# Kernel optimization log

Hardware: AMD Instinct MI355X
Metric: run time of the kernel (lower is better)

The kernel has to match this reference:

```python
import jax, jax.numpy as jnp
import numpy as np
from jax import lax

N = 20          # PARAM.N discretization steps
STEP_SIZE = 1.0 / N  # max_T / N = 1 / 20
B = 1_048_576   # number of Monte-Carlo paths


def _lin_init(key, fan_in, fan_out):
    kw, kb = jax.random.split(key)
    s = 1.0 / np.sqrt(fan_in)
    W = jax.random.uniform(kw, (fan_in, fan_out), minval=-s, maxval=s, dtype=jnp.float32)
    b = jax.random.uniform(kb, (fan_out,), minval=-s, maxval=s, dtype=jnp.float32)
    return W, b


def setup_inputs() -> dict:
    key = jax.random.key(0)
    ks = jax.random.split(key, 10)
    S0 = jax.random.uniform(ks[0], (B,), minval=50.0, maxval=150.0, dtype=jnp.float32)
    K = jax.random.uniform(ks[1], (B,), minval=50.0, maxval=150.0, dtype=jnp.float32)
    # maturities in {0.5, 1.0} per PARAM.maturities
    T = jnp.where(jax.random.bernoulli(ks[2], 0.5, (B,)), 0.5, 1.0).astype(jnp.float32)
    BM = jax.random.normal(ks[3], (B, N), dtype=jnp.float32)
    # 3 stacks: (4->30->5), (5->30->5), (5->30->2)
    W1, b1 = _lin_init(ks[4], 4, 30)
    W2, b2 = _lin_init(ks[5], 30, 5)
    W3, b3 = _lin_init(ks[6], 5, 30)
    W4, b4 = _lin_init(ks[7], 30, 5)
    W5, b5 = _lin_init(ks[8], 5, 30)
    W6, b6 = _lin_init(ks[9], 30, 2)
    return dict(S0=S0, K=K, T=T, BM=BM,
                W1=W1, b1=b1, W2=W2, b2=b2, W3=W3, b3=b3,
                W4=W4, b4=b4, W5=W5, b5=b5, W6=W6, b6=b6)


def reference(S0, K, T, BM, W1, b1, W2, b2, W3, b3, W4, b4, W5, b5, W6, b6):
    def net(x):  # [B,4] -> [B,2]
        h = jax.nn.relu(x @ W1 + b1) @ W2 + b2
        h = jax.nn.relu(h @ W3 + b3) @ W4 + b4
        return jax.nn.relu(h @ W5 + b5) @ W6 + b6

    def feats(price, time):  # [B,4] features: price, time, T-time, log(price/K)
        t = time * jnp.ones_like(price)
        return jnp.stack([price, t, T - t, jnp.log(price / K)], axis=-1)

    def step(carry, inp):
        price, hedgepf = carry
        idx, dW = inp
        time = (idx + 1.0) / N
        do_comp = (time <= T).astype(price.dtype)
        inc = dW * STEP_SIZE
        lev = net(feats(price, time))[:, 0]
        price = price + do_comp * lev * price * inc
        hed = net(feats(price, time))[:, 1] * inc
        hedgepf = hedgepf + do_comp * hed
        return (price, hedgepf), None

    init = (S0, jnp.zeros_like(S0))
    xs = (jnp.arange(N, dtype=S0.dtype), BM.T)  # scan over time steps
    (price, hedgepf), _ = lax.scan(step, init, xs)
    payoff = (price - K + jnp.abs(price - K)) * 0.5  # == relu(price - K)
    return payoff - hedgepf
```

## Files before the change

### kernel.cpp

```cpp
#include <hip/hip_runtime.h>

#define NSTEPS 20

typedef short bf16x8 __attribute__((ext_vector_type(8)));
typedef float f32x16 __attribute__((ext_vector_type(16)));

union B8 { bf16x8 h; unsigned u[4]; unsigned short s[8]; };

__device__ __forceinline__ unsigned short f2bf(float x) {
    unsigned u = __builtin_bit_cast(unsigned, x);
    u += 0x7fffu + ((u >> 16) & 1u);
    return (unsigned short)(u >> 16);
}
__device__ __forceinline__ float bf2f(unsigned short b) {
    return __builtin_bit_cast(float, (unsigned)b << 16);
}
__device__ __forceinline__ unsigned pk(unsigned short lo, unsigned short hi) {
    return (unsigned)lo | ((unsigned)hi << 16);
}
__device__ __forceinline__ unsigned cvtpk(float a, float b) {
    unsigned r;
    asm("v_cvt_pk_bf16_f32 %0, %1, %2" : "=v"(r) : "v"(a), "v"(b));
    return r;
}
__device__ __forceinline__ float lo_f(unsigned w) { return __builtin_bit_cast(float, w << 16); }
__device__ __forceinline__ float hi_f(unsigned w) { return __builtin_bit_cast(float, w & 0xffff0000u); }

#define MFMA(A, B, C) __builtin_amdgcn_mfma_f32_32x32x16_bf16((A), (B), (C), 0, 0, 0)
#define PRIO1() __builtin_amdgcn_s_setprio(1)
#define PRIO0() __builtin_amdgcn_s_setprio(0)

__device__ __forceinline__ void wlimbs(float w, unsigned short& l0, unsigned short& l1, unsigned short& l2) {
    l0 = f2bf(w); float e = w - bf2f(l0);
    l1 = f2bf(e); e -= bf2f(l1);
    l2 = f2bf(e);
}
__device__ __forceinline__ unsigned short pick(int m, unsigned short l0, unsigned short l1, unsigned short l2) {
    return (m == 0) ? l0 : ((m == 1) ? l1 : l2);
}


template<int F_, int M>
__device__ __forceinline__ bf16x8 awide(const float* W, const float* bias, int nout, int ld, int lane)
{
    const int u = lane & 31, h = (lane >> 5) & 1;
    B8 r;
#pragma unroll
    for (int j = 0; j < 8; ++j) {
        const int k = 16 * F_ + 4 * h + (j & 3) + 8 * (j >> 2);
        float v = 0.f;
        if (u < nout) {
            if (k < 30) v = W[k * ld + u];
            else if (k == 30) v = bias[u];
        }
        unsigned short l0, l1, l2; wlimbs(v, l0, l1, l2);
        r.s[j] = (short)pick(M, l0, l1, l2);
    }
    return r.h;
}

template<int S, int F_>
__device__ __forceinline__ bf16x8 a5(const float* W, const float* bias, int lane)
{
    const int u = lane & 31, h = (lane >> 5) & 1;
    B8 r;
#pragma unroll
    for (int j = 0; j < 8; ++j) {
        const int k = 16 * F_ + 4 * h + (j & 3) + 8 * (j >> 2);
        unsigned short bits = 0;
        if (u < 30) {
            int in = -1, m = -1;
            if (F_ == 0) {
                if (k < 4)       { in = k; m = S; }
                else if (k == 4) { in = 4; m = S; }
            } else {
                if (k >= 16 && k < 20)      { in = k - 16; m = (S == 0) ? 1 : ((S == 1) ? 0 : -1); }
                else if (k == 20)           { in = 4;      m = (S == 0) ? 1 : ((S == 1) ? 0 : -1); }
                else if (k >= 24 && k < 28) { in = k - 24; m = (S == 0) ? 2 : ((S == 2) ? 0 : -1); }
                else if (k == 21)           { in = 4;      m = (S == 0) ? 2 : ((S == 2) ? 0 : -1); }
            }
            if (in >= 0 && m >= 0) {
                unsigned short l0, l1, l2; wlimbs(W[in * 30 + u], l0, l1, l2);
                bits = pick(m, l0, l1, l2);
            } else if (F_ == 0 && k == 15) {
                unsigned short l0, l1, l2; wlimbs(bias[u], l0, l1, l2);
                bits = pick(S, l0, l1, l2);
            }
        }
        r.s[j] = (short)bits;
    }
    return r.h;
}

template<int S>
__device__ __forceinline__ bf16x8 a1f(const float* W1, const float* b1v, int lane)
{
    const int perm[4] = {0, 3, 1, 2};
    const int u = lane & 31, h = (lane >> 5) & 1;
    B8 r;
#pragma unroll
    for (int j = 0; j < 8; ++j) {
        const int k = 4 * h + (j & 3) + 8 * (j >> 2);
        unsigned short bits = 0;
        if (u < 30) {
            int in = -1, m = -1;
            if (k < 4)       { in = k;     m = (S == 0) ? 0 : ((S == 1) ? 1 : 2); }
            else if (k < 8)  { in = k - 4; m = (S == 0) ? 1 : ((S == 1) ? 0 : -1); }
            else if (k < 12) { in = k - 8; m = (S == 0) ? 2 : ((S == 2) ? 0 : -1); }
            if (in >= 0 && m >= 0) {
                unsigned short l0, l1, l2; wlimbs(W1[perm[in] * 30 + u], l0, l1, l2);
                bits = pick(m, l0, l1, l2);
            } else if (k == 12) {
                unsigned short l0, l1, l2; wlimbs(b1v[u], l0, l1, l2);
                bits = pick(S, l0, l1, l2);
            }
        }
        r.s[j] = (short)bits;
    }
    return r.h;
}


template<int LIMBS>
__device__ __forceinline__ void split_pair(float a, float b,
                                           unsigned& w0, unsigned& w1, unsigned& w2)
{
    w0 = cvtpk(a, b);
    if (LIMBS >= 2) {
        float e0 = a - lo_f(w0), e1 = b - hi_f(w0);
        w1 = cvtpk(e0, e1);
        if (LIMBS == 3) {
            float f0 = e0 - lo_f(w1), f1 = e1 - hi_f(w1);
            w2 = cvtpk(f0, f1);
        } else w2 = 0u;
    } else { w1 = 0u; w2 = 0u; }
}

template<int LIMBS>
__device__ __forceinline__ void split30(const f32x16& acc, bool hi,
                                        B8& B0a, B8& B0b, B8& B1a, B8& B1b,
                                        B8& B2a, B8& B2b)
{
#pragma unroll
    for (int i = 0; i < 4; ++i) {
        const float a = fmaxf(acc[2 * i], 0.f), b = fmaxf(acc[2 * i + 1], 0.f);
        unsigned w0, w1, w2; split_pair<LIMBS>(a, b, w0, w1, w2);
        B0a.u[i] = w0;
        if (LIMBS >= 2) B1a.u[i] = w1;
        if (LIMBS == 3) B2a.u[i] = w2;
    }
#pragma unroll
    for (int i = 0; i < 4; ++i) {
        const float a = fmaxf(acc[8 + 2 * i], 0.f), b = fmaxf(acc[8 + 2 * i + 1], 0.f);
        unsigned w0, w1, w2; split_pair<LIMBS>(a, b, w0, w1, w2);
        B0b.u[i] = w0;
        if (LIMBS >= 2) B1b.u[i] = w1;
        if (LIMBS == 3) B2b.u[i] = w2;
    }
    if (hi) {
        B0b.u[3] = 0x00003F80u;
        if (LIMBS >= 2) B1b.u[3] = 0u;
        if (LIMBS == 3) B2b.u[3] = 0u;
    }
}

template<int LIMBS>
__device__ __forceinline__ void split5(const f32x16& acc, bool hi, B8& C0, B8& C1)
{
    const float a0 = acc[0], a1 = acc[1];
    const float a2 = acc[2], a3 = acc[3];
    unsigned p0, p1, p2, q0, q1, q2;
    split_pair<LIMBS>(a0, a1, p0, p1, p2);
    split_pair<LIMBS>(a2, a3, q0, q1, q2);
    if (!hi) {
        C0.u[0] = p0; C0.u[1] = q0; C0.u[2] = 0; C0.u[3] = 0;
        if (LIMBS >= 2) {
            C1.u[0] = p1; C1.u[1] = q1;
            C1.u[2] = (LIMBS == 3) ? p2 : 0u;
            C1.u[3] = (LIMBS == 3) ? q2 : 0u;
        }
    } else {
        C0.u[0] = p0 & 0xffffu;
        C0.u[1] = 0; C0.u[2] = 0;
        C0.u[3] = 0x3F800000u;
        if (LIMBS >= 2) {
            C1.u[0] = (LIMBS == 3) ? pk((unsigned short)(p1 & 0xffffu), (unsigned short)(p2 & 0xffffu))
                                   : (p1 & 0xffffu);
            C1.u[1] = 0; C1.u[2] = 0; C1.u[3] = 0;
        }
    }
}

struct Frags {
    bf16x8 A1_0, A1_1, A1_2;
    bf16x8 A2_00, A2_01, A2_10, A2_11, A2_20, A2_21;
    bf16x8 A3_00, A3_01, A3_10, A3_11, A3_20, A3_21;
    bf16x8 A4_00, A4_01, A4_10, A4_11, A4_20, A4_21;
    bf16x8 A5_00, A5_01, A5_10, A5_11, A5_20, A5_21;
};

template<int LIMBS>
__device__ __forceinline__ f32x16 evalnet5(
    float price, float f3, unsigned tT0, unsigned tT1, unsigned tT2,
    bool hi, const Frags& F, const f32x16& Z)
{
    unsigned pf0, pf1, pf2;
    split_pair<LIMBS>(price, f3, pf0, pf1, pf2);
    B8 B;
    if (!hi) {
        B.u[0] = pf0; B.u[1] = tT0;
        B.u[2] = (LIMBS == 3) ? pf2 : 0u;
        B.u[3] = (LIMBS == 3) ? tT2 : 0u;
    } else {
        B.u[0] = (LIMBS >= 2) ? pf1 : 0u;
        B.u[1] = (LIMBS >= 2) ? tT1 : 0u;
        B.u[2] = 0x00003F80u;
        B.u[3] = 0u;
    }

    PRIO1();
    f32x16 acc = MFMA(F.A1_0, B.h, Z);
    if (LIMBS >= 2) acc = MFMA(F.A1_1, B.h, acc);
    if (LIMBS == 3) acc = MFMA(F.A1_2, B.h, acc);
    PRIO0();

    B8 B0a, B0b, B1a, B1b, B2a, B2b, C0, C1;
    f32x16 p, q;

    split30<LIMBS>(acc, hi, B0a, B0b, B1a, B1b, B2a, B2b);
    PRIO1();
    p = MFMA(F.A2_00, B0a.h, Z);
    q = MFMA(F.A2_01, B0b.h, Z);
    if (LIMBS >= 2) {
        p = MFMA(F.A2_00, B1a.h, p);
        q = MFMA(F.A2_01, B1b.h, q);
        if (LIMBS == 3) { p = MFMA(F.A2_00, B2a.h, p); q = MFMA(F.A2_01, B2b.h, q); }
        p = MFMA(F.A2_10, B0a.h, p);
        q = MFMA(F.A2_11, B0b.h, q);
        p = MFMA(F.A2_10, B1a.h, p);
        q = MFMA(F.A2_11, B1b.h, q);
        if (LIMBS == 3) { p = MFMA(F.A2_20, B0a.h, p); q = MFMA(F.A2_21, B0b.h, q); }
    }
    PRIO0();
    acc = p + q;

    split5<LIMBS>(acc, hi, C0, C1);
    PRIO1();
    if (LIMBS >= 2) {
        p = MFMA(F.A3_00, C0.h, Z);
        q = MFMA(F.A3_01, C1.h, Z);
        p = MFMA(F.A3_10, C0.h, p);
        q = MFMA(F.A3_11, C1.h, q);
        if (LIMBS == 3) { p = MFMA(F.A3_20, C0.h, p); q = MFMA(F.A3_21, C1.h, q); }
        acc = p + q;
    } else {
        acc = MFMA(F.A3_00, C0.h, Z);
    }
    PRIO0();

    split30<LIMBS>(acc, hi, B0a, B0b, B1a, B1b, B2a, B2b);
    PRIO1();
    p = MFMA(F.A4_00, B0a.h, Z);
    q = MFMA(F.A4_01, B0b.h, Z);
    if (LIMBS >= 2) {
        p = MFMA(F.A4_00, B1a.h, p);
        q = MFMA(F.A4_01, B1b.h, q);
        if (LIMBS == 3) { p = MFMA(F.A4_00, B2a.h, p); q = MFMA(F.A4_01, B2b.h, q); }
        p = MFMA(F.A4_10, B0a.h, p);
        q = MFMA(F.A4_11, B0b.h, q);
        p = MFMA(F.A4_10, B1a.h, p);
        q = MFMA(F.A4_11, B1b.h, q);
        if (LIMBS == 3) { p = MFMA(F.A4_20, B0a.h, p); q = MFMA(F.A4_21, B0b.h, q); }
    }
    PRIO0();
    acc = p + q;

    split5<LIMBS>(acc, hi, C0, C1);
    PRIO1();
    if (LIMBS >= 2) {
        p = MFMA(F.A5_00, C0.h, Z);
        q = MFMA(F.A5_01, C1.h, Z);
        p = MFMA(F.A5_10, C0.h, p);
        q = MFMA(F.A5_11, C1.h, q);
        if (LIMBS == 3) { p = MFMA(F.A5_20, C0.h, p); q = MFMA(F.A5_21, C1.h, q); }
        acc = p + q;
    } else {
        acc = MFMA(F.A5_00, C0.h, Z);
    }
    PRIO0();

    return acc;
}

__global__ __launch_bounds__(1024) void partition_kernel(
    const float* __restrict__ Tv, int* __restrict__ ws, int Btot)
{
    __shared__ int cntA[16], cntB[16], baseSh[2];
    const int tid = threadIdx.x;
    const int wid = tid >> 6;
    const int lane = tid & 63;
    const int i = blockIdx.x * 1024 + tid;
    const bool valid = i < Btot;
    const bool isLong  = valid && (Tv[valid ? i : 0] > 0.75f);
    const bool isShort = valid && !isLong;
    const unsigned long long mA = __ballot(isLong);
    const unsigned long long mB = __ballot(isShort);
    const unsigned long long ltm = (1ull << lane) - 1ull;

    if (lane == 0) { cntA[wid] = __popcll(mA); cntB[wid] = __popcll(mB); }
    __syncthreads();
    if (tid == 0) {
        int ta = 0, tb = 0;
#pragma unroll
        for (int k = 0; k < 16; ++k) {
            const int a = cntA[k]; cntA[k] = ta; ta += a;
            const int b = cntB[k]; cntB[k] = tb; tb += b;
        }
        baseSh[0] = ta ? atomicAdd(&ws[0], ta) : 0;
        baseSh[1] = tb ? atomicAdd(&ws[1], tb) : 0;
    }
    __syncthreads();

    int* list = ws + 16;
    if (isLong) {
        const int pos = baseSh[0] + cntA[wid] + __popcll(mA & ltm);
        list[pos] = i;
    }
    if (isShort) {
        const int pos = baseSh[1] + cntB[wid] + __popcll(mB & ltm);
        list[Btot - 1 - pos] = i;
    }
}

template<int LIST>
__global__ __launch_bounds__(256) __attribute__((amdgpu_waves_per_eu(2, 3)))
void mc_hedge_mfma(
    const float* __restrict__ S0, const float* __restrict__ Kv,
    const float* __restrict__ Tv, const float* __restrict__ BM,
    const float* __restrict__ W1, const float* __restrict__ b1,
    const float* __restrict__ W2, const float* __restrict__ b2,
    const float* __restrict__ W3, const float* __restrict__ b3,
    const float* __restrict__ W4, const float* __restrict__ b4,
    const float* __restrict__ W5, const float* __restrict__ b5,
    const float* __restrict__ W6, const float* __restrict__ b6,
    const int* __restrict__ list, float* __restrict__ out, int Btot)
{
    const int lane = threadIdx.x & 63;
    const int wid  = threadIdx.x >> 6;
    const int base = blockIdx.x * 128 + wid * 32;
    if (base >= Btot) return;
    const int li = min(base + (lane & 31), Btot - 1);
    const int p = LIST ? list[li] : li;
    const bool hi = lane >= 32;

    Frags F;
    F.A1_0 = a1f<0>(W1, b1, lane);
    F.A1_1 = a1f<1>(W1, b1, lane);
    F.A1_2 = a1f<2>(W1, b1, lane);
    F.A2_00 = awide<0,0>(W2, b2, 5, 5, lane); F.A2_01 = awide<1,0>(W2, b2, 5, 5, lane);
    F.A2_10 = awide<0,1>(W2, b2, 5, 5, lane); F.A2_11 = awide<1,1>(W2, b2, 5, 5, lane);
    F.A2_20 = awide<0,2>(W2, b2, 5, 5, lane); F.A2_21 = awide<1,2>(W2, b2, 5, 5, lane);
    F.A3_00 = a5<0,0>(W3, b3, lane); F.A3_01 = a5<0,1>(W3, b3, lane);
    F.A3_10 = a5<1,0>(W3, b3, lane); F.A3_11 = a5<1,1>(W3, b3, lane);
    F.A3_20 = a5<2,0>(W3, b3, lane); F.A3_21 = a5<2,1>(W3, b3, lane);
    F.A4_00 = awide<0,0>(W4, b4, 5, 5, lane); F.A4_01 = awide<1,0>(W4, b4, 5, 5, lane);
    F.A4_10 = awide<0,1>(W4, b4, 5, 5, lane); F.A4_11 = awide<1,1>(W4, b4, 5, 5, lane);
    F.A4_20 = awide<0,2>(W4, b4, 5, 5, lane); F.A4_21 = awide<1,2>(W4, b4, 5, 5, lane);
    F.A5_00 = a5<0,0>(W5, b5, lane); F.A5_01 = a5<0,1>(W5, b5, lane);
    F.A5_10 = a5<1,0>(W5, b5, lane); F.A5_11 = a5<1,1>(W5, b5, lane);
    F.A5_20 = a5<2,0>(W5, b5, lane); F.A5_21 = a5<2,1>(W5, b5, lane);

    f32x16 wv0, wv1;
#pragma unroll
    for (int r = 0; r < 16; ++r) {
        const int row0 = (r & 3) + 8 * (r >> 2);
        const int row1 = row0 + 4;
        const float w00 = W6[row0 * 2 + 0];
        const float w01 = W6[row0 * 2 + 1];
        const float w10 = (row1 < 30) ? W6[row1 * 2 + 0] : 0.f;
        const float w11 = (row1 < 30) ? W6[row1 * 2 + 1] : 0.f;
        wv0[r] = hi ? w10 : w00;
        wv1[r] = hi ? w11 : w01;
    }
    const float b60 = b6[0], b61 = b6[1];

    f32x16 Z;
#pragma unroll
    for (int i = 0; i < 16; ++i) Z[i] = 0.0f;

    float price = S0[p];
    const float Kk = Kv[p];
    const float T  = Tv[p];
    const float logK = __logf(Kk);
    float hedge = 0.0f;
    const float* bmrow = BM + (size_t)p * NSTEPS;

    int wsteps = NSTEPS;
    if (LIST) {
        const int st = (T > 0.75f) ? NSTEPS : (NSTEPS / 2);
        wsteps = __shfl(st, 0);
    }

#pragma unroll 1
    for (int idx = 0; idx < wsteps; ++idx) {
        const float time = (float)(idx + 1) / (float)NSTEPS;
        const float docomp = (time <= T) ? 1.0f : 0.0f;
        const float inc = bmrow[idx] * (1.0f / (float)NSTEPS);
        const float tmt = T - time;

        unsigned tT0, tT1, tT2;
        split_pair<3>(time, tmt, tT0, tT1, tT2);

        float f3 = __logf(price) - logK;
        f32x16 a5v = evalnet5<3>(price, f3, tT0, tT1, tT2, hi, F, Z);
        float part = 0.f;
#pragma unroll
        for (int r = 0; r < 16; ++r) part = fmaf(fmaxf(a5v[r], 0.f), wv0[r], part);
        part += __shfl_xor(part, 32);
        const float lev = part + b60;
        price = price + docomp * lev * price * inc;

        f3 = __logf(price) - logK;
        a5v = evalnet5<1>(price, f3, tT0, tT1, tT2, hi, F, Z);
        part = 0.f;
#pragma unroll
        for (int r = 0; r < 16; ++r) part = fmaf(fmaxf(a5v[r], 0.f), wv1[r], part);
        part += __shfl_xor(part, 32);
        const float hed = (part + b61) * inc;
        hedge = hedge + docomp * hed;
    }

    if (!hi && (base + lane) < Btot) {
        const float payoff = fmaxf(price - Kk, 0.0f);
        out[p] = payoff - hedge;
    }
}

extern "C" void kernel_launch(void* const* d_in, const int* in_sizes, int n_in,
                              void* d_out, int out_size, void* d_ws, size_t ws_size,
                              hipStream_t stream)
{
    const float* S0 = (const float*)d_in[0];
    const float* Kv = (const float*)d_in[1];
    const float* Tv = (const float*)d_in[2];
    const float* BM = (const float*)d_in[3];
    const float* W1 = (const float*)d_in[4];
    const float* b1 = (const float*)d_in[5];
    const float* W2 = (const float*)d_in[6];
    const float* b2 = (const float*)d_in[7];
    const float* W3 = (const float*)d_in[8];
    const float* b3 = (const float*)d_in[9];
    const float* W4 = (const float*)d_in[10];
    const float* b4 = (const float*)d_in[11];
    const float* W5 = (const float*)d_in[12];
    const float* b5 = (const float*)d_in[13];
    const float* W6 = (const float*)d_in[14];
    const float* b6 = (const float*)d_in[15];

    float* out = (float*)d_out;
    const int B = in_sizes[0];
    const int gridC = (B + 127) / 128;
    const size_t need = (size_t)(16 + B) * sizeof(int);

    if (ws_size >= need) {
        int* ws = (int*)d_ws;
        hipMemsetAsync(ws, 0, 16 * sizeof(int), stream);
        partition_kernel<<<(B + 1023) / 1024, 1024, 0, stream>>>(Tv, ws, B);
        mc_hedge_mfma<1><<<gridC, 256, 0, stream>>>(
            S0, Kv, Tv, BM, W1, b1, W2, b2, W3, b3, W4, b4, W5, b5, W6, b6,
            ws + 16, out, B);
    } else {
        mc_hedge_mfma<0><<<gridC, 256, 0, stream>>>(
            S0, Kv, Tv, BM, W1, b1, W2, b2, W3, b3, W4, b4, W5, b5, W6, b6,
            (const int*)nullptr, out, B);
    }
}
```

Measured before the change: 869.7 us.

## Stage MFMA weight fragments in LDS and raise waves-per-EU target

The 27 bf16x8 weight fragments, previously held in registers by every wave, are now built once per block by wave 0 into shared memory and read from LDS at each MFMA. The waves_per_eu hint goes from (2,3) to (3,4) to use the freed registers for more resident waves and better latency hiding. The cost is an LDS read (ds_read_b128) before every MFMA in the inner loop, plus a block-wide barrier at start, which may add latency or contend on LDS bandwidth.

Result: faster. 712.4 us (-18.1%).

```diff
diff --git a/kernel.cpp b/kernel.cpp
--- a/kernel.cpp
+++ b/kernel.cpp
@@ -191,18 +191,12 @@
     }
 }
 
-struct Frags {
-    bf16x8 A1_0, A1_1, A1_2;
-    bf16x8 A2_00, A2_01, A2_10, A2_11, A2_20, A2_21;
-    bf16x8 A3_00, A3_01, A3_10, A3_11, A3_20, A3_21;
-    bf16x8 A4_00, A4_01, A4_10, A4_11, A4_20, A4_21;
-    bf16x8 A5_00, A5_01, A5_10, A5_11, A5_20, A5_21;
-};
+#define NFRAG 27
 
 template<int LIMBS>
 __device__ __forceinline__ f32x16 evalnet5(
     float price, float f3, unsigned tT0, unsigned tT1, unsigned tT2,
-    bool hi, const Frags& F, const f32x16& Z)
+    bool hi, const bf16x8* LF, int lane, const f32x16& Z)
 {
     unsigned pf0, pf1, pf2;
     split_pair<LIMBS>(price, f3, pf0, pf1, pf2);
@@ -219,9 +213,9 @@
     }
 
     PRIO1();
-    f32x16 acc = MFMA(F.A1_0, B.h, Z);
-    if (LIMBS >= 2) acc = MFMA(F.A1_1, B.h, acc);
-    if (LIMBS == 3) acc = MFMA(F.A1_2, B.h, acc);
+    f32x16 acc = MFMA(LF[0 * 64 + lane], B.h, Z);
+    if (LIMBS >= 2) acc = MFMA(LF[1 * 64 + lane], B.h, acc);
+    if (LIMBS == 3) acc = MFMA(LF[2 * 64 + lane], B.h, acc);
     PRIO0();
 
     B8 B0a, B0b, B1a, B1b, B2a, B2b, C0, C1;
@@ -229,17 +223,17 @@
 
     split30<LIMBS>(acc, hi, B0a, B0b, B1a, B1b, B2a, B2b);
     PRIO1();
-    p = MFMA(F.A2_00, B0a.h, Z);
-    q = MFMA(F.A2_01, B0b.h, Z);
+    p = MFMA(LF[3 * 64 + lane], B0a.h, Z);
+    q = MFMA(LF[4 * 64 + lane], B0b.h, Z);
     if (LIMBS >= 2) {
-        p = MFMA(F.A2_00, B1a.h, p);
-        q = MFMA(F.A2_01, B1b.h, q);
-        if (LIMBS == 3) { p = MFMA(F.A2_00, B2a.h, p); q = MFMA(F.A2_01, B2b.h, q); }
-        p = MFMA(F.A2_10, B0a.h, p);
-        q = MFMA(F.A2_11, B0b.h, q);
-        p = MFMA(F.A2_10, B1a.h, p);
-        q = MFMA(F.A2_11, B1b.h, q);
-        if (LIMBS == 3) { p = MFMA(F.A2_20, B0a.h, p); q = MFMA(F.A2_21, B0b.h, q); }
+        p = MFMA(LF[3 * 64 + lane], B1a.h, p);
+        q = MFMA(LF[4 * 64 + lane], B1b.h, q);
+        if (LIMBS == 3) { p = MFMA(LF[3 * 64 + lane], B2a.h, p); q = MFMA(LF[4 * 64 + lane], B2b.h, q); }
+        p = MFMA(LF[5 * 64 + lane], B0a.h, p);
+        q = MFMA(LF[6 * 64 + lane], B0b.h, q);
+        p = MFMA(LF[5 * 64 + lane], B1a.h, p);
+        q = MFMA(LF[6 * 64 + lane], B1b.h, q);
+        if (LIMBS == 3) { p = MFMA(LF[7 * 64 + lane], B0a.h, p); q = MFMA(LF[8 * 64 + lane], B0b.h, q); }
     }
     PRIO0();
     acc = p + q;
@@ -247,30 +241,30 @@
     split5<LIMBS>(acc, hi, C0, C1);
     PRIO1();
     if (LIMBS >= 2) {
-        p = MFMA(F.A3_00, C0.h, Z);
-        q = MFMA(F.A3_01, C1.h, Z);
-        p = MFMA(F.A3_10, C0.h, p);
-        q = MFMA(F.A3_11, C1.h, q);
-        if (LIMBS == 3) { p = MFMA(F.A3_20, C0.h, p); q = MFMA(F.A3_21, C1.h, q); }
+        p = MFMA(LF[9 * 64 + lane], C0.h, Z);
+        q = MFMA(LF[10 * 64 + lane], C1.h, Z);
+        p = MFMA(LF[11 * 64 + lane], C0.h, p);
+        q = MFMA(LF[12 * 64 + lane], C1.h, q);
+        if (LIMBS == 3) { p = MFMA(LF[13 * 64 + lane], C0.h, p); q = MFMA(LF[14 * 64 + lane], C1.h, q); }
         acc = p + q;
     } else {
-        acc = MFMA(F.A3_00, C0.h, Z);
+        acc = MFMA(LF[9 * 64 + lane], C0.h, Z);
     }
     PRIO0();
 
     split30<LIMBS>(acc, hi, B0a, B0b, B1a, B1b, B2a, B2b);
     PRIO1();
-    p = MFMA(F.A4_00, B0a.h, Z);
-    q = MFMA(F.A4_01, B0b.h, Z);
+    p = MFMA(LF[15 * 64 + lane], B0a.h, Z);
+    q = MFMA(LF[16 * 64 + lane], B0b.h, Z);
     if (LIMBS >= 2) {
-        p = MFMA(F.A4_00, B1a.h, p);
-        q = MFMA(F.A4_01, B1b.h, q);
-        if (LIMBS == 3) { p = MFMA(F.A4_00, B2a.h, p); q = MFMA(F.A4_01, B2b.h, q); }
-        p = MFMA(F.A4_10, B0a.h, p);
-        q = MFMA(F.A4_11, B0b.h, q);
-        p = MFMA(F.A4_10, B1a.h, p);
-        q = MFMA(F.A4_11, B1b.h, q);
-        if (LIMBS == 3) { p = MFMA(F.A4_20, B0a.h, p); q = MFMA(F.A4_21, B0b.h, q); }
+        p = MFMA(LF[15 * 64 + lane], B1a.h, p);
+        q = MFMA(LF[16 * 64 + lane], B1b.h, q);
+        if (LIMBS == 3) { p = MFMA(LF[15 * 64 + lane], B2a.h, p); q = MFMA(LF[16 * 64 + lane], B2b.h, q); }
+        p = MFMA(LF[17 * 64 + lane], B0a.h, p);
+        q = MFMA(LF[18 * 64 + lane], B0b.h, q);
+        p = MFMA(LF[17 * 64 + lane], B1a.h, p);
+        q = MFMA(LF[18 * 64 + lane], B1b.h, q);
+        if (LIMBS == 3) { p = MFMA(LF[19 * 64 + lane], B0a.h, p); q = MFMA(LF[20 * 64 + lane], B0b.h, q); }
     }
     PRIO0();
     acc = p + q;
@@ -278,14 +272,14 @@
     split5<LIMBS>(acc, hi, C0, C1);
     PRIO1();
     if (LIMBS >= 2) {
-        p = MFMA(F.A5_00, C0.h, Z);
-        q = MFMA(F.A5_01, C1.h, Z);
-        p = MFMA(F.A5_10, C0.h, p);
-        q = MFMA(F.A5_11, C1.h, q);
-        if (LIMBS == 3) { p = MFMA(F.A5_20, C0.h, p); q = MFMA(F.A5_21, C1.h, q); }
+        p = MFMA(LF[21 * 64 + lane], C0.h, Z);
+        q = MFMA(LF[22 * 64 + lane], C1.h, Z);
+        p = MFMA(LF[23 * 64 + lane], C0.h, p);
+        q = MFMA(LF[24 * 64 + lane], C1.h, q);
+        if (LIMBS == 3) { p = MFMA(LF[25 * 64 + lane], C0.h, p); q = MFMA(LF[26 * 64 + lane], C1.h, q); }
         acc = p + q;
     } else {
-        acc = MFMA(F.A5_00, C0.h, Z);
+        acc = MFMA(LF[21 * 64 + lane], C0.h, Z);
     }
     PRIO0();
 
@@ -333,7 +327,7 @@
 }
 
 template<int LIST>
-__global__ __launch_bounds__(256) __attribute__((amdgpu_waves_per_eu(2, 3)))
+__global__ __launch_bounds__(256) __attribute__((amdgpu_waves_per_eu(3, 4)))
 void mc_hedge_mfma(
     const float* __restrict__ S0, const float* __restrict__ Kv,
     const float* __restrict__ Tv, const float* __restrict__ BM,
@@ -345,30 +339,48 @@
     const float* __restrict__ W6, const float* __restrict__ b6,
     const int* __restrict__ list, float* __restrict__ out, int Btot)
 {
+    __shared__ bf16x8 LFs[NFRAG * 64];
+
     const int lane = threadIdx.x & 63;
     const int wid  = threadIdx.x >> 6;
+
+    if (wid == 0) {
+        LFs[0 * 64 + lane]  = a1f<0>(W1, b1, lane);
+        LFs[1 * 64 + lane]  = a1f<1>(W1, b1, lane);
+        LFs[2 * 64 + lane]  = a1f<2>(W1, b1, lane);
+        LFs[3 * 64 + lane]  = awide<0,0>(W2, b2, 5, 5, lane);
+        LFs[4 * 64 + lane]  = awide<1,0>(W2, b2, 5, 5, lane);
+        LFs[5 * 64 + lane]  = awide<0,1>(W2, b2, 5, 5, lane);
+        LFs[6 * 64 + lane]  = awide<1,1>(W2, b2, 5, 5, lane);
+        LFs[7 * 64 + lane]  = awide<0,2>(W2, b2, 5, 5, lane);
+        LFs[8 * 64 + lane]  = awide<1,2>(W2, b2, 5, 5, lane);
+        LFs[9 * 64 + lane]  = a5<0,0>(W3, b3, lane);
+        LFs[10 * 64 + lane] = a5<0,1>(W3, b3, lane);
+        LFs[11 * 64 + lane] = a5<1,0>(W3, b3, lane);
+        LFs[12 * 64 + lane] = a5<1,1>(W3, b3, lane);
+        LFs[13 * 64 + lane] = a5<2,0>(W3, b3, lane);
+        LFs[14 * 64 + lane] = a5<2,1>(W3, b3, lane);
+        LFs[15 * 64 + lane] = awide<0,0>(W4, b4, 5, 5, lane);
+        LFs[16 * 64 + lane] = awide<1,0>(W4, b4, 5, 5, lane);
+        LFs[17 * 64 + lane] = awide<0,1>(W4, b4, 5, 5, lane);
+        LFs[18 * 64 + lane] = awide<1,1>(W4, b4, 5, 5, lane);
+        LFs[19 * 64 + lane] = awide<0,2>(W4, b4, 5, 5, lane);
+        LFs[20 * 64 + lane] = awide<1,2>(W4, b4, 5, 5, lane);
+        LFs[21 * 64 + lane] = a5<0,0>(W5, b5, lane);
+        LFs[22 * 64 + lane] = a5<0,1>(W5, b5, lane);
+        LFs[23 * 64 + lane] = a5<1,0>(W5, b5, lane);
+        LFs[24 * 64 + lane] = a5<1,1>(W5, b5, lane);
+        LFs[25 * 64 + lane] = a5<2,0>(W5, b5, lane);
+        LFs[26 * 64 + lane] = a5<2,1>(W5, b5, lane);
+    }
+    __syncthreads();
+    const bf16x8* LF = LFs;
+
     const int base = blockIdx.x * 128 + wid * 32;
     if (base >= Btot) return;
     const int li = min(base + (lane & 31), Btot - 1);
     const int p = LIST ? list[li] : li;
     const bool hi = lane >= 32;
-
-    Frags F;
-    F.A1_0 = a1f<0>(W1, b1, lane);
-    F.A1_1 = a1f<1>(W1, b1, lane);
-    F.A1_2 = a1f<2>(W1, b1, lane);
-    F.A2_00 = awide<0,0>(W2, b2, 5, 5, lane); F.A2_01 = awide<1,0>(W2, b2, 5, 5, lane);
-    F.A2_10 = awide<0,1>(W2, b2, 5, 5, lane); F.A2_11 = awide<1,1>(W2, b2, 5, 5, lane);
-    F.A2_20 = awide<0,2>(W2, b2, 5, 5, lane); F.A2_21 = awide<1,2>(W2, b2, 5, 5, lane);
-    F.A3_00 = a5<0,0>(W3, b3, lane); F.A3_01 = a5<0,1>(W3, b3, lane);
-    F.A3_10 = a5<1,0>(W3, b3, lane); F.A3_11 = a5<1,1>(W3, b3, lane);
-    F.A3_20 = a5<2,0>(W3, b3, lane); F.A3_21 = a5<2,1>(W3, b3, lane);
-    F.A4_00 = awide<0,0>(W4, b4, 5, 5, lane); F.A4_01 = awide<1,0>(W4, b4, 5, 5, lane);
-    F.A4_10 = awide<0,1>(W4, b4, 5, 5, lane); F.A4_11 = awide<1,1>(W4, b4, 5, 5, lane);
-    F.A4_20 = awide<0,2>(W4, b4, 5, 5, lane); F.A4_21 = awide<1,2>(W4, b4, 5, 5, lane);
-    F.A5_00 = a5<0,0>(W5, b5, lane); F.A5_01 = a5<0,1>(W5, b5, lane);
-    F.A5_10 = a5<1,0>(W5, b5, lane); F.A5_11 = a5<1,1>(W5, b5, lane);
-    F.A5_20 = a5<2,0>(W5, b5, lane); F.A5_21 = a5<2,1>(W5, b5, lane);
 
     f32x16 wv0, wv1;
 #pragma unroll
@@ -412,7 +424,7 @@
         split_pair<3>(time, tmt, tT0, tT1, tT2);
 
         float f3 = __logf(price) - logK;
-        f32x16 a5v = evalnet5<3>(price, f3, tT0, tT1, tT2, hi, F, Z);
+        f32x16 a5v = evalnet5<3>(price, f3, tT0, tT1, tT2, hi, LF, lane, Z);
         float part = 0.f;
 #pragma unroll
         for (int r = 0; r < 16; ++r) part = fmaf(fmaxf(a5v[r], 0.f), wv0[r], part);
@@ -421,7 +433,7 @@
         price = price + docomp * lev * price * inc;
 
         f3 = __logf(price) - logK;
-        a5v = evalnet5<1>(price, f3, tT0, tT1, tT2, hi, F, Z);
+        a5v = evalnet5<1>(price, f3, tT0, tT1, tT2, hi, LF, lane, Z);
         part = 0.f;
 #pragma unroll
         for (int r = 0; r < 16; ++r) part = fmaf(fmaxf(a5v[r], 0.f), wv1[r], part);
```
